# Kernel tuning notes

Hardware: AMD Instinct MI355X
Metric: run time of the kernel (lower is better)

Reference implementation:

```python
import jax, jax.numpy as jnp
import numpy as np

B, S, H, I = 4, 2048, 2048, 8192
LN_EPS = 1e-6  # DeepSpeed inference layer-norm epsilon


def setup_inputs() -> dict:
    key = jax.random.key(0)
    ks = jax.random.split(key, 10)
    return {
        "input": jax.random.normal(ks[0], (B, S, H), dtype=jnp.float32),
        "residual": jax.random.normal(ks[1], (B, S, H), dtype=jnp.float32),
        "residual_norm": jax.random.normal(ks[2], (B, S, H), dtype=jnp.float32),
        "bias": jax.random.normal(ks[3], (H,), dtype=jnp.float32) * 0.02,
        "gamma": jnp.ones((H,), dtype=jnp.float32) + jax.random.normal(ks[4], (H,), dtype=jnp.float32) * 0.02,
        "beta": jax.random.normal(ks[5], (H,), dtype=jnp.float32) * 0.02,
        "inter_w": jax.random.normal(ks[6], (H, I), dtype=jnp.float32) * 0.02,
        "inter_b": jax.random.normal(ks[7], (I,), dtype=jnp.float32) * 0.02,
        "output_w": jax.random.normal(ks[8], (I, H), dtype=jnp.float32) * 0.02,
        "output_b": jax.random.normal(ks[9], (H,), dtype=jnp.float32) * 0.02,
    }


def reference(input, residual, residual_norm, bias, gamma, beta,
              inter_w, inter_b, output_w, output_b):
    # --- mlp_gemm_func (pre-LN path, attn_nw is not None) ---
    # Fused: residual_add = attention_output + attention_bias + residual
    residual_add = input + residual + bias                    # [B,S,H]
    # LayerNorm over hidden dim
    mu = jnp.mean(residual_add, axis=-1, keepdims=True)
    var = jnp.mean(jnp.square(residual_add - mu), axis=-1, keepdims=True)
    ln = (residual_add - mu) * jax.lax.rsqrt(var + LN_EPS) * gamma + beta
    # GEMM + bias + GeLU, then second GEMM
    h = jax.nn.gelu(jnp.einsum("bsh,hi->bsi", ln, inter_w) + inter_b,
                    approximate=False)                        # [B,S,I]
    out = jnp.einsum("bsi,ih->bsh", h, output_w)              # [B,S,H]
    # --- residual_add_func (pre-LN, mlp_after_attn): mlp_out + residual_add + final_bias ---
    return out + residual_add + output_b
```

## Files before the change

kernel.cpp:

```cpp
#include <hip/hip_runtime.h>

typedef __attribute__((ext_vector_type(8))) __bf16 bf16x8;
typedef __attribute__((ext_vector_type(4))) float f32x4;

#define AS1(p) ((const __attribute__((address_space(1))) void*)(uintptr_t)(p))
#define AS3(p) ((__attribute__((address_space(3))) void*)(uint32_t)(uintptr_t)(p))
#define GLD16(gp, lp) __builtin_amdgcn_global_load_lds(AS1(gp), AS3(lp), 16, 0, 0)

static constexpr int Bb = 4, Ss = 2048, Hh = 2048, Ih = 8192;
static constexpr int Mm = Bb * Ss;

__device__ __forceinline__ float gelu_exact(float x) {
    return 0.5f * x * (1.0f + erff(x * 0.70710678118654752440f));
}

__global__ __launch_bounds__(256) void transpose_cvt(const float* __restrict__ src,
                                                     __bf16* __restrict__ dst,
                                                     int R, int C) {
    __shared__ float tile[32][33];
    const int tx = threadIdx.x, ty = threadIdx.y;
    const int cB = blockIdx.x * 32, rB = blockIdx.y * 32;
#pragma unroll
    for (int i = 0; i < 4; ++i)
        tile[ty + i * 8][tx] = src[(size_t)(rB + ty + i * 8) * C + cB + tx];
    __syncthreads();
#pragma unroll
    for (int i = 0; i < 4; ++i)
        dst[(size_t)(cB + ty + i * 8) * R + rB + tx] = (__bf16)tile[tx][ty + i * 8];
}

__global__ __launch_bounds__(256) void fused_ln(const float* __restrict__ input,
                                                const float* __restrict__ residual,
                                                const float* __restrict__ bias,
                                                const float* __restrict__ gamma,
                                                const float* __restrict__ beta,
                                                __bf16* __restrict__ lnb,
                                                __bf16* __restrict__ rab) {
    const int row = blockIdx.x;
    const int tid = threadIdx.x;
    const size_t base = (size_t)row * Hh;
    const int e = tid * 8;

    float4 x0 = *(const float4*)(input + base + e);
    float4 x1 = *(const float4*)(input + base + e + 4);
    float4 r0 = *(const float4*)(residual + base + e);
    float4 r1 = *(const float4*)(residual + base + e + 4);
    float4 b0 = *(const float4*)(bias + e);
    float4 b1 = *(const float4*)(bias + e + 4);

    float s[8];
    s[0] = x0.x + r0.x + b0.x; s[1] = x0.y + r0.y + b0.y;
    s[2] = x0.z + r0.z + b0.z; s[3] = x0.w + r0.w + b0.w;
    s[4] = x1.x + r1.x + b1.x; s[5] = x1.y + r1.y + b1.y;
    s[6] = x1.z + r1.z + b1.z; s[7] = x1.w + r1.w + b1.w;

    float sum = 0.f, sq = 0.f;
#pragma unroll
    for (int j = 0; j < 8; ++j) { sum += s[j]; sq += s[j] * s[j]; }
#pragma unroll
    for (int o = 32; o > 0; o >>= 1) {
        sum += __shfl_xor(sum, o);
        sq  += __shfl_xor(sq, o);
    }
    __shared__ float red[8];
    const int wv = tid >> 6, ln_ = tid & 63;
    if (ln_ == 0) { red[wv] = sum; red[4 + wv] = sq; }
    __syncthreads();
    sum = red[0] + red[1] + red[2] + red[3];
    sq  = red[4] + red[5] + red[6] + red[7];

    const float mu   = sum * (1.0f / Hh);
    const float var  = sq * (1.0f / Hh) - mu * mu;
    const float rstd = rsqrtf(var + 1e-6f);

    float4 g0 = *(const float4*)(gamma + e);
    float4 g1 = *(const float4*)(gamma + e + 4);
    float4 t0 = *(const float4*)(beta + e);
    float4 t1 = *(const float4*)(beta + e + 4);
    float g[8] = {g0.x, g0.y, g0.z, g0.w, g1.x, g1.y, g1.z, g1.w};
    float t[8] = {t0.x, t0.y, t0.z, t0.w, t1.x, t1.y, t1.z, t1.w};

    bf16x8 lv, rv;
#pragma unroll
    for (int j = 0; j < 8; ++j) {
        rv[j] = (__bf16)s[j];
        lv[j] = (__bf16)((s[j] - mu) * rstd * g[j] + t[j]);
    }
    *(bf16x8*)(lnb + base + e) = lv;
    *(bf16x8*)(rab + base + e) = rv;
}


#define CFENCE asm volatile("" ::: "memory")
#define BAR()  do { CFENCE; __builtin_amdgcn_s_barrier(); CFENCE; } while (0)

__device__ __forceinline__ void ldA4(const char* p0, const char* p1, const int mhOff,
                                     bf16x8 (&af)[4][2]) {
#pragma unroll
    for (int m = 0; m < 4; ++m) {
        af[m][0] = *(const bf16x8*)(p0 + mhOff + m * 2048);
        af[m][1] = *(const bf16x8*)(p1 + mhOff + m * 2048);
    }
}
__device__ __forceinline__ void ldB2(const char* p0, const char* p1, const int nhOff,
                                     bf16x8 (&bf)[2][2]) {
#pragma unroll
    for (int n = 0; n < 2; ++n) {
        bf[n][0] = *(const bf16x8*)(p0 + nhOff + n * 2048);
        bf[n][1] = *(const bf16x8*)(p1 + nhOff + n * 2048);
    }
}
template <int MH, int NH>
__device__ __forceinline__ void mfmaQ(const bf16x8 (&a)[4][2], const bf16x8 (&b)[2][2],
                                      f32x4 (&acc)[8][4]) {
#pragma unroll
    for (int m = 0; m < 4; ++m)
#pragma unroll
        for (int n = 0; n < 2; ++n)
#pragma unroll
            for (int ks = 0; ks < 2; ++ks)
                acc[MH * 4 + m][NH * 2 + n] = __builtin_amdgcn_mfma_f32_16x16x32_bf16(
                    a[m][ks], b[n][ks], acc[MH * 4 + m][NH * 2 + n], 0, 0, 0);
}
__device__ __forceinline__ void stage2(const __bf16* src, __bf16* dst, const size_t row64) {
    GLD16(src, dst);
    GLD16(src + row64, dst + 4096);
}

template <int MODE>
__global__ __launch_bounds__(512, 2) void gemm256(const __bf16* __restrict__ A,
                                                  const __bf16* __restrict__ Bt,
                                                  const float* __restrict__ bias,
                                                  const __bf16* __restrict__ rab,
                                                  __bf16* __restrict__ outH,
                                                  float* __restrict__ outF,
                                                  int M, int N, int K) {
    __shared__ __align__(128) __bf16 lds[2 * 4 * 128 * 64];

    const int tid = threadIdx.x;
    const int nbx = N >> 8;
    const int nwg = gridDim.x;
    const int cpx = nwg >> 3;
    const int bid = blockIdx.x;
    const int swz = (bid & 7) * cpx + (bid >> 3);
    const int by = swz / nbx, bx = swz - by * nbx;
    const int mBase = by << 8, nBase = bx << 8;

    const int wave = tid >> 6, lane = tid & 63;
    const int wr = wave >> 2, wc = wave & 3;

    const int NT = K >> 6;
    const int NI = NT >> 1;

    char* ldsc = (char*)lds;
    const int laneCol0 = (((lane >> 4) << 4)) ^ ((lane & 7) << 4);
    const int laneCol1 = laneCol0 ^ 64;
    const int aLaneR = (lane & 15) << 7;
    const int bLaneR = (((wc & 1) << 6) + (lane & 15)) << 7;
    const char* pA[2][2] = {
        {ldsc + (0 * 4 + wr) * 16384 + aLaneR + laneCol0,
         ldsc + (0 * 4 + wr) * 16384 + aLaneR + laneCol1},
        {ldsc + (1 * 4 + wr) * 16384 + aLaneR + laneCol0,
         ldsc + (1 * 4 + wr) * 16384 + aLaneR + laneCol1}};
    const char* pB[2][2] = {
        {ldsc + (0 * 4 + 2 + (wc >> 1)) * 16384 + bLaneR + laneCol0,
         ldsc + (0 * 4 + 2 + (wc >> 1)) * 16384 + bLaneR + laneCol1},
        {ldsc + (1 * 4 + 2 + (wc >> 1)) * 16384 + bLaneR + laneCol0,
         ldsc + (1 * 4 + 2 + (wc >> 1)) * 16384 + bLaneR + laneCol1}};

    const int srow = tid >> 3;
    const int scol = ((tid & 7) ^ (srow & 7)) << 3;
    const __bf16* aSt = A + (size_t)(mBase + srow) * K + scol;
    const __bf16* bSt = Bt + (size_t)(nBase + srow) * K + scol;
    __bf16* lw = lds + tid * 8;
    const size_t row64 = (size_t)64 * K;
    const size_t row128 = (size_t)128 * K;

#define STA(buf, h, t) stage2(aSt + (h) * row128 + (size_t)(t) * 64, lw + ((buf) * 4 + (h)) * 8192, row64)
#define STB(buf, h, t) stage2(bSt + (h) * row128 + (size_t)(t) * 64, lw + ((buf) * 4 + 2 + (h)) * 8192, row64)

    f32x4 acc[8][4] = {};
    bf16x8 a0v[4][2], a1v[4][2], b0v[2][2], b1v[2][2];

    STA(0, 0, 0); STA(0, 1, 0); STB(0, 0, 0); STB(0, 1, 0);
    STB(1, 0, 1); STB(1, 1, 1);
    asm volatile("s_waitcnt vmcnt(4)" ::: "memory");
    BAR();

#define TILE(bi, S1, S2, S3, S4, BOUND)                                        \
    ldA4(pA[bi][0], pA[bi][1], 0, a0v);                                        \
    ldB2(pB[bi][0], pB[bi][1], 0, b0v);                                        \
    ldA4(pA[bi][0], pA[bi][1], 8192, a1v);                                     \
    S1;                                                                        \
    BAR();                                                                     \
    asm volatile("s_waitcnt lgkmcnt(8)" ::: "memory");                         \
    __builtin_amdgcn_s_setprio(1);                                             \
    mfmaQ<0, 0>(a0v, b0v, acc);                                                \
    __builtin_amdgcn_s_setprio(0);                                             \
    BAR();                                                                     \
    ldB2(pB[bi][0], pB[bi][1], 4096, b1v);                                     \
    S2;                                                                        \
    BAR();                                                                     \
    asm volatile("s_waitcnt lgkmcnt(4)" ::: "memory");                         \
    __builtin_amdgcn_s_setprio(1);                                             \
    mfmaQ<1, 0>(a1v, b0v, acc);                                                \
    __builtin_amdgcn_s_setprio(0);                                             \
    BAR();                                                                     \
    S3;                                                                        \
    BAR();                                                                     \
    asm volatile("s_waitcnt lgkmcnt(0)" ::: "memory");                         \
    __builtin_amdgcn_s_setprio(1);                                             \
    mfmaQ<1, 1>(a1v, b1v, acc);                                                \
    __builtin_amdgcn_s_setprio(0);                                             \
    BAR();                                                                     \
    S4;                                                                        \
    BAR();                                                                     \
    __builtin_amdgcn_s_setprio(1);                                             \
    mfmaQ<0, 1>(a0v, b1v, acc);                                                \
    __builtin_amdgcn_s_setprio(0);                                             \
    BOUND;                                                                     \
    BAR();

    for (int i = 0; i < NI; ++i) {
        const int t0 = 2 * i, t1 = 2 * i + 1;
        const bool pf0 = (t0 + 2 < NT);
        const bool pf1 = (t1 + 2 < NT);

        TILE(0,
             STA(1, 0, t1),
             STA(1, 1, t1),
             if (pf0) STB(0, 0, t0 + 2),
             if (pf0) STB(0, 1, t0 + 2),
             if (pf0) { asm volatile("s_waitcnt vmcnt(4)" ::: "memory"); }
             else     { asm volatile("s_waitcnt vmcnt(0)" ::: "memory"); })

        TILE(1,
             if (pf0) STA(0, 0, t0 + 2),
             if (pf0) STA(0, 1, t0 + 2),
             if (pf1) STB(1, 0, t1 + 2),
             if (pf1) STB(1, 1, t1 + 2),
             if (pf1) { asm volatile("s_waitcnt vmcnt(4)" ::: "memory"); })
    }
#undef TILE

    const int r0 = mBase + wr * 128 + ((lane >> 4) << 2);
    const int c0 = nBase + wc * 64 + (lane & 15);
    float bb[4];
#pragma unroll
    for (int nf = 0; nf < 4; ++nf) bb[nf] = bias[c0 + nf * 16];
#pragma unroll
    for (int mf = 0; mf < 8; ++mf) {
        const int row = r0 + mf * 16;
#pragma unroll
        for (int nf = 0; nf < 4; ++nf) {
            const int col = c0 + nf * 16;
#pragma unroll
            for (int j = 0; j < 4; ++j) {
                const size_t idx = (size_t)(row + j) * N + col;
                const float v = acc[mf][nf][j] + bb[nf];
                if (MODE == 0) {
                    outH[idx] = (__bf16)gelu_exact(v);
                } else {
                    outF[idx] = v + (float)rab[idx];
                }
            }
        }
    }
#undef STA
#undef STB
}

extern "C" void kernel_launch(void* const* d_in, const int* in_sizes, int n_in,
                              void* d_out, int out_size, void* d_ws, size_t ws_size,
                              hipStream_t stream) {
    const float* input    = (const float*)d_in[0];
    const float* residual = (const float*)d_in[1];
    const float* bias     = (const float*)d_in[3];
    const float* gamma    = (const float*)d_in[4];
    const float* beta     = (const float*)d_in[5];
    const float* inter_w  = (const float*)d_in[6];
    const float* inter_b  = (const float*)d_in[7];
    const float* output_w = (const float*)d_in[8];
    const float* output_b = (const float*)d_in[9];
    float* out = (float*)d_out;

    __bf16* w1t  = (__bf16*)d_ws;
    __bf16* w2t  = w1t + (size_t)Ih * Hh;
    __bf16* lnb  = w2t + (size_t)Hh * Ih;
    __bf16* rab  = lnb + (size_t)Mm * Hh;
    __bf16* hbuf = rab + (size_t)Mm * Hh;

    transpose_cvt<<<dim3(Ih / 32, Hh / 32), dim3(32, 8), 0, stream>>>(inter_w, w1t, Hh, Ih);
    transpose_cvt<<<dim3(Hh / 32, Ih / 32), dim3(32, 8), 0, stream>>>(output_w, w2t, Ih, Hh);

    fused_ln<<<Mm, 256, 0, stream>>>(input, residual, bias, gamma, beta, lnb, rab);

    gemm256<0><<<dim3((Mm / 256) * (Ih / 256)), 512, 0, stream>>>(
        lnb, w1t, inter_b, nullptr, hbuf, nullptr, Mm, Ih, Hh);

    gemm256<1><<<dim3((Mm / 256) * (Hh / 256)), 512, 0, stream>>>(
        hbuf, w2t, output_b, rab, nullptr, out, Mm, Hh, Ih);
}
```

Baseline: 692.7 us.

## Restructure GEMM main loop into a double-buffered pipeline with fewer barriers

Rewrites the GEMM K-loop schedule. Both A and B tiles are now prefetched two steps ahead, and the next tile's first LDS fragments are read during the current tile's last MFMA quadrant. The MFMA quadrant order changes, barriers per tile drop from eight to two, and the last iterations are peeled so prefetch conditionals are gone. The aim is to overlap LDS reads and global-to-LDS staging with MFMA work and cut synchronisation stalls. The cost is tighter reasoning about LDS buffer reuse hazards and larger vmcnt windows.

```diff
diff --git a/kernel.cpp b/kernel.cpp
--- a/kernel.cpp
+++ b/kernel.cpp
@@ -93,6 +93,12 @@
 
 #define CFENCE asm volatile("" ::: "memory")
 #define BAR()  do { CFENCE; __builtin_amdgcn_s_barrier(); CFENCE; } while (0)
+#define SP1 __builtin_amdgcn_s_setprio(1)
+#define SP0 __builtin_amdgcn_s_setprio(0)
+#define VM8 asm volatile("s_waitcnt vmcnt(8)" ::: "memory")
+#define VM4 asm volatile("s_waitcnt vmcnt(4)" ::: "memory")
+#define VM0 asm volatile("s_waitcnt vmcnt(0)" ::: "memory")
+#define NOPS ((void)0)
 
 __device__ __forceinline__ void ldA4(const char* p0, const char* p1, const int mhOff,
                                      bf16x8 (&af)[4][2]) {
@@ -178,69 +184,41 @@
 
 #define STA(buf, h, t) stage2(aSt + (h) * row128 + (size_t)(t) * 64, lw + ((buf) * 4 + (h)) * 8192, row64)
 #define STB(buf, h, t) stage2(bSt + (h) * row128 + (size_t)(t) * 64, lw + ((buf) * 4 + 2 + (h)) * 8192, row64)
+#define STGB(P, T) do { STB(P, 0, T); STB(P, 1, T); } while (0)
+#define STGA(P, T) do { STA(P, 0, T); STA(P, 1, T); } while (0)
+#define RDN(NP) do { ldB2(pB[NP][0], pB[NP][1], 0, b0v); \
+                     ldA4(pA[NP][0], pA[NP][1], 0, a0v); } while (0)
 
     f32x4 acc[8][4] = {};
     bf16x8 a0v[4][2], a1v[4][2], b0v[2][2], b1v[2][2];
 
-    STA(0, 0, 0); STA(0, 1, 0); STB(0, 0, 0); STB(0, 1, 0);
-    STB(1, 0, 1); STB(1, 1, 1);
-    asm volatile("s_waitcnt vmcnt(4)" ::: "memory");
+    STGB(0, 0); STGA(0, 0);
+    STGB(1, 1); STGA(1, 1);
+    VM8;
     BAR();
-
-#define TILE(bi, S1, S2, S3, S4, BOUND)                                        \
-    ldA4(pA[bi][0], pA[bi][1], 0, a0v);                                        \
-    ldB2(pB[bi][0], pB[bi][1], 0, b0v);                                        \
-    ldA4(pA[bi][0], pA[bi][1], 8192, a1v);                                     \
-    S1;                                                                        \
-    BAR();                                                                     \
-    asm volatile("s_waitcnt lgkmcnt(8)" ::: "memory");                         \
-    __builtin_amdgcn_s_setprio(1);                                             \
-    mfmaQ<0, 0>(a0v, b0v, acc);                                                \
-    __builtin_amdgcn_s_setprio(0);                                             \
-    BAR();                                                                     \
-    ldB2(pB[bi][0], pB[bi][1], 4096, b1v);                                     \
-    S2;                                                                        \
-    BAR();                                                                     \
-    asm volatile("s_waitcnt lgkmcnt(4)" ::: "memory");                         \
-    __builtin_amdgcn_s_setprio(1);                                             \
-    mfmaQ<1, 0>(a1v, b0v, acc);                                                \
-    __builtin_amdgcn_s_setprio(0);                                             \
-    BAR();                                                                     \
-    S3;                                                                        \
-    BAR();                                                                     \
-    asm volatile("s_waitcnt lgkmcnt(0)" ::: "memory");                         \
-    __builtin_amdgcn_s_setprio(1);                                             \
-    mfmaQ<1, 1>(a1v, b1v, acc);                                                \
-    __builtin_amdgcn_s_setprio(0);                                             \
-    BAR();                                                                     \
-    S4;                                                                        \
-    BAR();                                                                     \
-    __builtin_amdgcn_s_setprio(1);                                             \
-    mfmaQ<0, 1>(a0v, b1v, acc);                                                \
-    __builtin_amdgcn_s_setprio(0);                                             \
-    BOUND;                                                                     \
-    BAR();
-
-    for (int i = 0; i < NI; ++i) {
-        const int t0 = 2 * i, t1 = 2 * i + 1;
-        const bool pf0 = (t0 + 2 < NT);
-        const bool pf1 = (t1 + 2 < NT);
-
-        TILE(0,
-             STA(1, 0, t1),
-             STA(1, 1, t1),
-             if (pf0) STB(0, 0, t0 + 2),
-             if (pf0) STB(0, 1, t0 + 2),
-             if (pf0) { asm volatile("s_waitcnt vmcnt(4)" ::: "memory"); }
-             else     { asm volatile("s_waitcnt vmcnt(0)" ::: "memory"); })
-
-        TILE(1,
-             if (pf0) STA(0, 0, t0 + 2),
-             if (pf0) STA(0, 1, t0 + 2),
-             if (pf1) STB(1, 0, t1 + 2),
-             if (pf1) STB(1, 1, t1 + 2),
-             if (pf1) { asm volatile("s_waitcnt vmcnt(4)" ::: "memory"); })
-    }
+    RDN(0);
+
+#define TILE(P, NP, STAGEB, GATE, STAGEA, NEXTRD)          \
+    SP1; mfmaQ<0, 0>(a0v, b0v, acc); SP0;                  \
+    ldB2(pB[P][0], pB[P][1], 4096, b1v);                   \
+    SP1; mfmaQ<0, 1>(a0v, b1v, acc); SP0;                  \
+    ldA4(pA[P][0], pA[P][1], 8192, a1v);                   \
+    BAR();                                                 \
+    SP1; mfmaQ<1, 1>(a1v, b1v, acc); SP0;                  \
+    STAGEB;                                                \
+    GATE;                                                  \
+    BAR();                                                 \
+    SP1; mfmaQ<1, 0>(a1v, b0v, acc); SP0;                  \
+    NEXTRD;                                                \
+    STAGEA;
+
+    for (int i = 0; i < NI - 1; ++i) {
+        const int t2a = 2 * i + 2, t2b = 2 * i + 3;
+        TILE(0, 1, STGB(0, t2a), VM4, STGA(0, t2a), RDN(1))
+        TILE(1, 0, STGB(1, t2b), VM4, STGA(1, t2b), RDN(0))
+    }
+    TILE(0, 1, NOPS, VM0, NOPS, RDN(1))
+    TILE(1, 0, NOPS, NOPS, NOPS, NOPS)
 #undef TILE
 
     const int r0 = mBase + wr * 128 + ((lane >> 4) << 2);
@@ -268,6 +246,9 @@
     }
 #undef STA
 #undef STB
+#undef STGB
+#undef STGA
+#undef RDN
 }
 
 extern "C" void kernel_launch(void* const* d_in, const int* in_sizes, int n_in,
```

New measurement: 731.8 us. +5.7%, slower.
